# Performance work log

Measured on AMD Instinct MI355X. Metric: run time of the kernel, lower is better.

The kernel has to match this reference:

```python
import jax, jax.numpy as jnp
import numpy as np

B_SZ, SEQ, D_MODEL, N_STATE = 4, 2048, 768, 16


def setup_inputs() -> dict:
    key = jax.random.key(0)
    ks = jax.random.split(key, 8)
    s = 1.0 / np.sqrt(D_MODEL)
    x = jax.random.normal(ks[0], (B_SZ, SEQ, D_MODEL), dtype=jnp.float32)
    W1 = jax.random.uniform(ks[1], (D_MODEL, D_MODEL), jnp.float32, -s, s)
    b1 = jax.random.uniform(ks[2], (D_MODEL,), jnp.float32, -s, s)
    W2 = jax.random.uniform(ks[3], (D_MODEL, N_STATE), jnp.float32, -s, s)
    b2 = jax.random.uniform(ks[4], (N_STATE,), jnp.float32, -s, s)
    W3 = jax.random.uniform(ks[5], (D_MODEL, N_STATE), jnp.float32, -s, s)
    b3 = jax.random.uniform(ks[6], (N_STATE,), jnp.float32, -s, s)
    # A: xavier_uniform over (d_model, state_size)
    a_bound = np.sqrt(6.0 / (D_MODEL + N_STATE))
    A = jax.random.uniform(ks[7], (D_MODEL, N_STATE), jnp.float32, -a_bound, a_bound)
    return {"x": x, "W1": W1, "b1": b1, "W2": W2, "b2": b2, "W3": W3, "b3": b3, "A": A}


def reference(x, W1, b1, W2, b2, W3, b3, A):
    # Input-dependent projections
    Bm = x @ W2 + b2                     # [b, l, n]
    Cm = x @ W3 + b3                     # [b, l, n]
    delta = jax.nn.softplus(x @ W1 + b1)  # [b, l, d]
    # Discretization (S6)
    dB = delta[..., None] * Bm[:, :, None, :]                 # [b, l, d, n]
    dA = jnp.exp(jnp.einsum('bld,dn->bldn', delta, A))        # [b, l, d, n]
    # Source initializes h to zeros, so the dA*h term vanishes (no recurrence).
    h0 = jnp.zeros_like(dB)
    h = dA * h0 + x[..., None] * dB                            # [b, l, d, n]
    y = jnp.einsum('bln,bldn->bld', Cm, h)                     # [b, l, d]
    return y
```

## Files before the change

kernel.cpp:

```cpp
#include <hip/hip_runtime.h>
#include <hip/hip_bf16.h>
#include <math.h>


#define M_ROWS 8192
#define DM 768
#define NS 16

typedef short bf16x8 __attribute__((ext_vector_type(8)));
typedef float f32x4 __attribute__((ext_vector_type(4)));

__device__ __forceinline__ unsigned short f2bf(float f) {
    union { float f; unsigned u; } v; v.f = f;
    unsigned r = v.u + 0x7FFF + ((v.u >> 16) & 1);
    return (unsigned short)(r >> 16);
}
__device__ __forceinline__ float bf2f(unsigned short h) {
    union { unsigned u; float f; } v; v.u = ((unsigned)h) << 16; return v.f;
}
__device__ __forceinline__ void async16(const void* g, void* l) {
    __builtin_amdgcn_global_load_lds(
        (const __attribute__((address_space(1))) void*)g,
        (__attribute__((address_space(3))) void*)l,
        16, 0, 0);
}

__global__ __launch_bounds__(256) void prep_kernel(
    const float* __restrict__ x,
    const float* __restrict__ W1,
    const float* __restrict__ W2,
    const float* __restrict__ W3,
    unsigned short* __restrict__ xb,
    unsigned short* __restrict__ w1t,
    unsigned short* __restrict__ w23t)
{
    __shared__ float tile[32][33];
    const int bid = blockIdx.x;
    const int tid = threadIdx.x;
    if (bid < 32) {
        const int n = bid, i = n >> 1;
        const float* src = (n & 1) ? W3 : W2;
        #pragma unroll
        for (int e = 0; e < 3; ++e) {
            int k = e * 256 + tid;
            w23t[n * DM + k] = f2bf(src[k * NS + i]);
        }
    } else if (bid < 608) {
        const int b2i = bid - 32;
        const int n0 = (b2i % 24) * 32, k0 = (b2i / 24) * 32;
        const int tx = tid & 31, ty = tid >> 5;
        #pragma unroll
        for (int i = 0; i < 4; ++i) {
            int k = ty + i * 8;
            tile[k][tx] = W1[(k0 + k) * DM + n0 + tx];
        }
        __syncthreads();
        #pragma unroll
        for (int i = 0; i < 4; ++i) {
            int n = ty + i * 8;
            w1t[(n0 + n) * DM + k0 + tx] = f2bf(tile[tx][n]);
        }
    } else {
        int i = (bid - 608) * 256 + tid;
        float4 v = ((const float4*)x)[i];
        ushort4 o;
        o.x = f2bf(v.x); o.y = f2bf(v.y); o.z = f2bf(v.z); o.w = f2bf(v.w);
        ((ushort4*)xb)[i] = o;
    }
}

__global__ __launch_bounds__(256) void sgemm_kernel(
    const unsigned short* __restrict__ xb,
    const unsigned short* __restrict__ w23t,
    const float* __restrict__ b2, const float* __restrict__ b3,
    float* __restrict__ s_out)
{
    __shared__ unsigned short Al[64 * 64];
    __shared__ unsigned short Bl[32 * 64];
    const int m0 = blockIdx.x * 64;
    const int tid = threadIdx.x, lane = tid & 63, wave = tid >> 6;
    const int l15 = lane & 15, quad = lane >> 4;

    f32x4 acc[2];
    acc[0] = (f32x4){0.f,0.f,0.f,0.f};
    acc[1] = (f32x4){0.f,0.f,0.f,0.f};

    for (int k0 = 0; k0 < DM; k0 += 64) {
        #pragma unroll
        for (int i = 0; i < 2; ++i) {
            int ch = tid + i * 256;
            int r = ch >> 3, jg = (ch & 7) ^ (r & 7);
            async16(xb + (m0 + r) * DM + k0 + jg * 8, Al + ch * 8);
        }
        {
            int ch = tid;
            int r = ch >> 3, jg = (ch & 7) ^ (r & 7);
            async16(w23t + r * DM + k0 + jg * 8, Bl + ch * 8);
        }
        __syncthreads();
        #pragma unroll
        for (int kk = 0; kk < 2; ++kk) {
            int rr = wave * 16 + l15;
            int ja = (kk * 4 + quad) ^ (rr & 7);
            bf16x8 af = *(const bf16x8*)(Al + rr * 64 + ja * 8);
            #pragma unroll
            for (int t = 0; t < 2; ++t) {
                int rb = t * 16 + l15;
                int jb = (kk * 4 + quad) ^ (rb & 7);
                bf16x8 bfr = *(const bf16x8*)(Bl + rb * 64 + jb * 8);
                acc[t] = __builtin_amdgcn_mfma_f32_16x16x32_bf16(
                    af, bfr, acc[t], 0, 0, 0);
            }
        }
        __syncthreads();
    }

    float sacc[4] = {0.f, 0.f, 0.f, 0.f};
    #pragma unroll
    for (int t = 0; t < 2; ++t) {
        int p = t * 8 + (l15 >> 1);
        float bB = b2[p], bC = b3[p];
        #pragma unroll
        for (int r = 0; r < 4; ++r) {
            float v = acc[t][r];
            float pv = __shfl_xor(v, 1, 64);
            float term = (l15 & 1) ? (pv + bB) * (v + bC)
                                   : (v + bB) * (pv + bC);
            sacc[r] += term;
        }
    }
    #pragma unroll
    for (int r = 0; r < 4; ++r) {
        sacc[r] += __shfl_xor(sacc[r], 1, 64);
        sacc[r] += __shfl_xor(sacc[r], 2, 64);
        sacc[r] += __shfl_xor(sacc[r], 4, 64);
        sacc[r] += __shfl_xor(sacc[r], 8, 64);
    }
    if (l15 == 0) {
        #pragma unroll
        for (int r = 0; r < 4; ++r)
            s_out[m0 + wave * 16 + quad * 4 + r] = 0.5f * sacc[r];
    }
}

__global__ __launch_bounds__(256) void gemm_fused_kernel(
    const unsigned short* __restrict__ xb,
    const unsigned short* __restrict__ w1t,
    const float* __restrict__ b1,
    const float* __restrict__ s_arr,
    float* __restrict__ y)
{
    __shared__ unsigned short Al[128 * 64];
    __shared__ unsigned short Bl[64 * 64];
    const int b = blockIdx.x;
    const int c = b & 7, j = b >> 3;
    const int m0 = (c * 8 + j / 12) * 128;
    const int n0 = (j % 12) * 64;
    const int tid  = threadIdx.x;
    const int lane = tid & 63;
    const int wave = tid >> 6;
    const int wm = wave >> 1, wn = wave & 1;
    const int l15 = lane & 15, quad = lane >> 4;

    f32x4 acc[4][2];
    #pragma unroll
    for (int i = 0; i < 4; ++i)
        #pragma unroll
        for (int jj = 0; jj < 2; ++jj)
            acc[i][jj] = (f32x4){0.f, 0.f, 0.f, 0.f};

    for (int k0 = 0; k0 < DM; k0 += 64) {
        #pragma unroll
        for (int i = 0; i < 4; ++i) {
            int ch = tid + i * 256;
            int r = ch >> 3, jg = (ch & 7) ^ (r & 7);
            async16(xb + (m0 + r) * DM + k0 + jg * 8, Al + ch * 8);
        }
        #pragma unroll
        for (int i = 0; i < 2; ++i) {
            int ch = tid + i * 256;
            int r = ch >> 3, jg = (ch & 7) ^ (r & 7);
            async16(w1t + (n0 + r) * DM + k0 + jg * 8, Bl + ch * 8);
        }
        __syncthreads();

        #pragma unroll
        for (int kk = 0; kk < 2; ++kk) {
            bf16x8 bfr[2];
            #pragma unroll
            for (int jj = 0; jj < 2; ++jj) {
                int rb = wn * 32 + jj * 16 + l15;
                int jb = (kk * 4 + quad) ^ (rb & 7);
                bfr[jj] = *(const bf16x8*)(Bl + rb * 64 + jb * 8);
            }
            #pragma unroll
            for (int i = 0; i < 4; ++i) {
                int rr = wm * 64 + i * 16 + l15;
                int ja = (kk * 4 + quad) ^ (rr & 7);
                bf16x8 af = *(const bf16x8*)(Al + rr * 64 + ja * 8);
                #pragma unroll
                for (int jj = 0; jj < 2; ++jj)
                    acc[i][jj] = __builtin_amdgcn_mfma_f32_16x16x32_bf16(
                        af, bfr[jj], acc[i][jj], 0, 0, 0);
            }
        }
        __syncthreads();
    }

    #pragma unroll
    for (int i = 0; i < 4; ++i) {
        const int rowbase = m0 + wm * 64 + i * 16 + quad * 4;
        float4 s4 = *(const float4*)(s_arr + rowbase);
        #pragma unroll
        for (int jj = 0; jj < 2; ++jj) {
            int gcol = n0 + wn * 32 + jj * 16 + l15;
            float bias = b1[gcol];
            #pragma unroll
            for (int r = 0; r < 4; ++r) {
                int grow = rowbase + r;
                float v = acc[i][jj][r] + bias;
                float sp = (v > 20.f) ? v : log1pf(__expf(v));
                float xv = bf2f(xb[grow * DM + gcol]);
                float sv = (r == 0) ? s4.x : (r == 1) ? s4.y : (r == 2) ? s4.z : s4.w;
                y[grow * DM + gcol] = xv * sp * sv;
            }
        }
    }
}

extern "C" void kernel_launch(void* const* d_in, const int* in_sizes, int n_in,
                              void* d_out, int out_size, void* d_ws, size_t ws_size,
                              hipStream_t stream) {
    const float* x  = (const float*)d_in[0];
    const float* W1 = (const float*)d_in[1];
    const float* b1 = (const float*)d_in[2];
    const float* W2 = (const float*)d_in[3];
    const float* b2 = (const float*)d_in[4];
    const float* W3 = (const float*)d_in[5];
    const float* b3 = (const float*)d_in[6];
    float* y = (float*)d_out;

    unsigned short* xb   = (unsigned short*)d_ws;
    unsigned short* w1t  = (unsigned short*)((char*)d_ws + 12582912);
    unsigned short* w23t = (unsigned short*)((char*)d_ws + 13762560);
    float*          sarr = (float*)((char*)d_ws + 13811712);

    prep_kernel<<<6752, 256, 0, stream>>>(x, W1, W2, W3, xb, w1t, w23t);
    sgemm_kernel<<<128, 256, 0, stream>>>(xb, w23t, b2, b3, sarr);
    gemm_fused_kernel<<<768, 256, 0, stream>>>(xb, w1t, b1, sarr, y);
}
```

Measured before the change: 136.7 us.

## Double-buffer LDS tiles in main GEMM to overlap loads with MFMA

Splits the A and B shared-memory tiles of the fused W1 GEMM into two buffers. The first K-slice is loaded before the loop, and each iteration prefetches the next slice into the other buffer while MFMAs run on the current one. This leaves one barrier per iteration instead of two. The cost is doubled LDS use per block (48 KB), which may limit how many blocks fit on a CU. It also adds unused index variables.

```diff
diff --git a/kernel.cpp b/kernel.cpp
--- a/kernel.cpp
+++ b/kernel.cpp
@@ -150,8 +150,8 @@
     const float* __restrict__ s_arr,
     float* __restrict__ y)
 {
-    __shared__ unsigned short Al[128 * 64];
-    __shared__ unsigned short Bl[64 * 64];
+    __shared__ unsigned short Al[2][128 * 64];
+    __shared__ unsigned short Bl[2][64 * 64];
     const int b = blockIdx.x;
     const int c = b & 7, j = b >> 3;
     const int m0 = (c * 8 + j / 12) * 128;
@@ -162,6 +162,8 @@
     const int wm = wave >> 1, wn = wave & 1;
     const int l15 = lane & 15, quad = lane >> 4;
 
+    const int rA0 = tid >> 3, jA0 = (tid & 7) ^ (rA0 & 7);
+
     f32x4 acc[4][2];
     #pragma unroll
     for (int i = 0; i < 4; ++i)
@@ -169,20 +171,42 @@
         for (int jj = 0; jj < 2; ++jj)
             acc[i][jj] = (f32x4){0.f, 0.f, 0.f, 0.f};
 
-    for (int k0 = 0; k0 < DM; k0 += 64) {
+    {
+        const int k0 = 0;
         #pragma unroll
         for (int i = 0; i < 4; ++i) {
             int ch = tid + i * 256;
             int r = ch >> 3, jg = (ch & 7) ^ (r & 7);
-            async16(xb + (m0 + r) * DM + k0 + jg * 8, Al + ch * 8);
+            async16(xb + (m0 + r) * DM + k0 + jg * 8, &Al[0][ch * 8]);
         }
         #pragma unroll
         for (int i = 0; i < 2; ++i) {
             int ch = tid + i * 256;
             int r = ch >> 3, jg = (ch & 7) ^ (r & 7);
-            async16(w1t + (n0 + r) * DM + k0 + jg * 8, Bl + ch * 8);
-        }
-        __syncthreads();
+            async16(w1t + (n0 + r) * DM + k0 + jg * 8, &Bl[0][ch * 8]);
+        }
+    }
+
+    for (int step = 0; step < DM / 64; ++step) {
+        const int cur = step & 1;
+        __syncthreads();
+
+        if (step + 1 < DM / 64) {
+            const int k0 = (step + 1) * 64;
+            const int nxt = cur ^ 1;
+            #pragma unroll
+            for (int i = 0; i < 4; ++i) {
+                int ch = tid + i * 256;
+                int r = ch >> 3, jg = (ch & 7) ^ (r & 7);
+                async16(xb + (m0 + r) * DM + k0 + jg * 8, &Al[nxt][ch * 8]);
+            }
+            #pragma unroll
+            for (int i = 0; i < 2; ++i) {
+                int ch = tid + i * 256;
+                int r = ch >> 3, jg = (ch & 7) ^ (r & 7);
+                async16(w1t + (n0 + r) * DM + k0 + jg * 8, &Bl[nxt][ch * 8]);
+            }
+        }
 
         #pragma unroll
         for (int kk = 0; kk < 2; ++kk) {
@@ -191,20 +215,19 @@
             for (int jj = 0; jj < 2; ++jj) {
                 int rb = wn * 32 + jj * 16 + l15;
                 int jb = (kk * 4 + quad) ^ (rb & 7);
-                bfr[jj] = *(const bf16x8*)(Bl + rb * 64 + jb * 8);
+                bfr[jj] = *(const bf16x8*)(&Bl[cur][rb * 64 + jb * 8]);
             }
             #pragma unroll
             for (int i = 0; i < 4; ++i) {
                 int rr = wm * 64 + i * 16 + l15;
                 int ja = (kk * 4 + quad) ^ (rr & 7);
-                bf16x8 af = *(const bf16x8*)(Al + rr * 64 + ja * 8);
+                bf16x8 af = *(const bf16x8*)(&Al[cur][rr * 64 + ja * 8]);
                 #pragma unroll
                 for (int jj = 0; jj < 2; ++jj)
                     acc[i][jj] = __builtin_amdgcn_mfma_f32_16x16x32_bf16(
                         af, bfr[jj], acc[i][jj], 0, 0, 0);
             }
         }
-        __syncthreads();
     }
 
     #pragma unroll
@@ -226,6 +249,7 @@
             }
         }
     }
+    (void)rA0; (void)jA0;
 }
 
 extern "C" void kernel_launch(void* const* d_in, const int* in_sizes, int n_in,
```

Result: no change. 135.8 us (-0.7%).

## Fuse x conversion and state GEMM into prep; use two-wave 128x64 GEMM blocks

Applied to the files above, without the earlier changes.

The x-to-bf16 conversion and the small B/C projection GEMM now run in one kernel. Each block reads fp32 x directly, converts it in registers, writes xb and feeds it to MFMA while loading W2/W3 columns into LDS, which removes one launch and the extra xb read. The main GEMM now uses 128 threads (2 waves), each wave computing a 64x64 subtile with 16 accumulators and launch bounds of 3 blocks per SM, so each LDS B fragment is reused more. The risks are uncoalesced strided W2/W3 loads in every prep block, only 128 blocks doing the heavy x conversion, and fewer waves per block in the main GEMM to hide latency.

```diff
diff --git a/kernel.cpp b/kernel.cpp
--- a/kernel.cpp
+++ b/kernel.cpp
@@ -25,28 +25,99 @@
         16, 0, 0);
 }
 
-__global__ __launch_bounds__(256) void prep_kernel(
+__global__ __launch_bounds__(256) void prep_s_kernel(
     const float* __restrict__ x,
     const float* __restrict__ W1,
-    const float* __restrict__ W2,
-    const float* __restrict__ W3,
+    const float* __restrict__ W2, const float* __restrict__ b2,
+    const float* __restrict__ W3, const float* __restrict__ b3,
     unsigned short* __restrict__ xb,
     unsigned short* __restrict__ w1t,
-    unsigned short* __restrict__ w23t)
+    float* __restrict__ s_out)
 {
+    __shared__ unsigned short Bl[32 * 64];
     __shared__ float tile[32][33];
     const int bid = blockIdx.x;
     const int tid = threadIdx.x;
-    if (bid < 32) {
-        const int n = bid, i = n >> 1;
-        const float* src = (n & 1) ? W3 : W2;
-        #pragma unroll
-        for (int e = 0; e < 3; ++e) {
-            int k = e * 256 + tid;
-            w23t[n * DM + k] = f2bf(src[k * NS + i]);
-        }
-    } else if (bid < 608) {
-        const int b2i = bid - 32;
+
+    if (bid < 128) {
+        const int wave = tid >> 6, lane = tid & 63;
+        const int l15 = lane & 15, quad = lane >> 4;
+        const int rowbase = bid * 64 + wave * 16;
+        const int row = rowbase + l15;
+
+        const int sn = tid & 31;
+        const int skg = tid >> 5;
+        const float* wsrc = ((sn & 1) ? W3 : W2) + (sn >> 1);
+        const int sswz = skg ^ (sn & 7);
+
+        f32x4 acc[2];
+        acc[0] = (f32x4){0.f,0.f,0.f,0.f};
+        acc[1] = (f32x4){0.f,0.f,0.f,0.f};
+
+        for (int k0 = 0; k0 < DM; k0 += 64) {
+            {
+                float v[8];
+                #pragma unroll
+                for (int jj = 0; jj < 8; ++jj)
+                    v[jj] = wsrc[(k0 + skg * 8 + jj) * NS];
+                bf16x8 bv;
+                #pragma unroll
+                for (int jj = 0; jj < 8; ++jj)
+                    bv[jj] = (short)f2bf(v[jj]);
+                *(bf16x8*)(Bl + sn * 64 + sswz * 8) = bv;
+            }
+            __syncthreads();
+            #pragma unroll
+            for (int kk = 0; kk < 2; ++kk) {
+                const int kq = k0 + kk * 32 + quad * 8;
+                const float4* xp = (const float4*)(x + row * DM + kq);
+                float4 a0 = xp[0], a1 = xp[1];
+                bf16x8 af;
+                af[0] = (short)f2bf(a0.x); af[1] = (short)f2bf(a0.y);
+                af[2] = (short)f2bf(a0.z); af[3] = (short)f2bf(a0.w);
+                af[4] = (short)f2bf(a1.x); af[5] = (short)f2bf(a1.y);
+                af[6] = (short)f2bf(a1.z); af[7] = (short)f2bf(a1.w);
+                *(bf16x8*)(xb + row * DM + kq) = af;
+                #pragma unroll
+                for (int t = 0; t < 2; ++t) {
+                    int rb = t * 16 + l15;
+                    int jb = (kk * 4 + quad) ^ (rb & 7);
+                    bf16x8 bfr = *(const bf16x8*)(Bl + rb * 64 + jb * 8);
+                    acc[t] = __builtin_amdgcn_mfma_f32_16x16x32_bf16(
+                        af, bfr, acc[t], 0, 0, 0);
+                }
+            }
+            __syncthreads();
+        }
+
+        float sacc[4] = {0.f, 0.f, 0.f, 0.f};
+        #pragma unroll
+        for (int t = 0; t < 2; ++t) {
+            int p = t * 8 + (l15 >> 1);
+            float bB = b2[p], bC = b3[p];
+            #pragma unroll
+            for (int r = 0; r < 4; ++r) {
+                float v = acc[t][r];
+                float pv = __shfl_xor(v, 1, 64);
+                float term = (l15 & 1) ? (pv + bB) * (v + bC)
+                                       : (v + bB) * (pv + bC);
+                sacc[r] += term;
+            }
+        }
+        #pragma unroll
+        for (int r = 0; r < 4; ++r) {
+            sacc[r] += __shfl_xor(sacc[r], 1, 64);
+            sacc[r] += __shfl_xor(sacc[r], 2, 64);
+            sacc[r] += __shfl_xor(sacc[r], 4, 64);
+            sacc[r] += __shfl_xor(sacc[r], 8, 64);
+        }
+        if (l15 == 0) {
+            #pragma unroll
+            for (int r = 0; r < 4; ++r)
+                s_out[rowbase + quad * 4 + r] = 0.5f * sacc[r];
+        }
+    } else {
+        const int b2i = bid - 128;
         const int n0 = (b2i % 24) * 32, k0 = (b2i / 24) * 32;
         const int tx = tid & 31, ty = tid >> 5;
         #pragma unroll
@@ -60,90 +131,10 @@
             int n = ty + i * 8;
             w1t[(n0 + n) * DM + k0 + tx] = f2bf(tile[tx][n]);
         }
-    } else {
-        int i = (bid - 608) * 256 + tid;
-        float4 v = ((const float4*)x)[i];
-        ushort4 o;
-        o.x = f2bf(v.x); o.y = f2bf(v.y); o.z = f2bf(v.z); o.w = f2bf(v.w);
-        ((ushort4*)xb)[i] = o;
     }
 }
 
-__global__ __launch_bounds__(256) void sgemm_kernel(
-    const unsigned short* __restrict__ xb,
-    const unsigned short* __restrict__ w23t,
-    const float* __restrict__ b2, const float* __restrict__ b3,
-    float* __restrict__ s_out)
-{
-    __shared__ unsigned short Al[64 * 64];
-    __shared__ unsigned short Bl[32 * 64];
-    const int m0 = blockIdx.x * 64;
-    const int tid = threadIdx.x, lane = tid & 63, wave = tid >> 6;
-    const int l15 = lane & 15, quad = lane >> 4;
-
-    f32x4 acc[2];
-    acc[0] = (f32x4){0.f,0.f,0.f,0.f};
-    acc[1] = (f32x4){0.f,0.f,0.f,0.f};
-
-    for (int k0 = 0; k0 < DM; k0 += 64) {
-        #pragma unroll
-        for (int i = 0; i < 2; ++i) {
-            int ch = tid + i * 256;
-            int r = ch >> 3, jg = (ch & 7) ^ (r & 7);
-            async16(xb + (m0 + r) * DM + k0 + jg * 8, Al + ch * 8);
-        }
-        {
-            int ch = tid;
-            int r = ch >> 3, jg = (ch & 7) ^ (r & 7);
-            async16(w23t + r * DM + k0 + jg * 8, Bl + ch * 8);
-        }
-        __syncthreads();
-        #pragma unroll
-        for (int kk = 0; kk < 2; ++kk) {
-            int rr = wave * 16 + l15;
-            int ja = (kk * 4 + quad) ^ (rr & 7);
-            bf16x8 af = *(const bf16x8*)(Al + rr * 64 + ja * 8);
-            #pragma unroll
-            for (int t = 0; t < 2; ++t) {
-                int rb = t * 16 + l15;
-                int jb = (kk * 4 + quad) ^ (rb & 7);
-                bf16x8 bfr = *(const bf16x8*)(Bl + rb * 64 + jb * 8);
-                acc[t] = __builtin_amdgcn_mfma_f32_16x16x32_bf16(
-                    af, bfr, acc[t], 0, 0, 0);
-            }
-        }
-        __syncthreads();
-    }
-
-    float sacc[4] = {0.f, 0.f, 0.f, 0.f};
-    #pragma unroll
-    for (int t = 0; t < 2; ++t) {
-        int p = t * 8 + (l15 >> 1);
-        float bB = b2[p], bC = b3[p];
-        #pragma unroll
-        for (int r = 0; r < 4; ++r) {
-            float v = acc[t][r];
-            float pv = __shfl_xor(v, 1, 64);
-            float term = (l15 & 1) ? (pv + bB) * (v + bC)
-                                   : (v + bB) * (pv + bC);
-            sacc[r] += term;
-        }
-    }
-    #pragma unroll
-    for (int r = 0; r < 4; ++r) {
-        sacc[r] += __shfl_xor(sacc[r], 1, 64);
-        sacc[r] += __shfl_xor(sacc[r], 2, 64);
-        sacc[r] += __shfl_xor(sacc[r], 4, 64);
-        sacc[r] += __shfl_xor(sacc[r], 8, 64);
-    }
-    if (l15 == 0) {
-        #pragma unroll
-        for (int r = 0; r < 4; ++r)
-            s_out[m0 + wave * 16 + quad * 4 + r] = 0.5f * sacc[r];
-    }
-}
-
-__global__ __launch_bounds__(256) void gemm_fused_kernel(
+__global__ __launch_bounds__(128, 3) void gemm_fused_kernel(
     const unsigned short* __restrict__ xb,
     const unsigned short* __restrict__ w1t,
     const float* __restrict__ b1,
@@ -158,27 +149,26 @@
     const int n0 = (j % 12) * 64;
     const int tid  = threadIdx.x;
     const int lane = tid & 63;
-    const int wave = tid >> 6;
-    const int wm = wave >> 1, wn = wave & 1;
+    const int w    = tid >> 6;
     const int l15 = lane & 15, quad = lane >> 4;
 
-    f32x4 acc[4][2];
+    f32x4 acc[4][4];
     #pragma unroll
     for (int i = 0; i < 4; ++i)
         #pragma unroll
-        for (int jj = 0; jj < 2; ++jj)
+        for (int jj = 0; jj < 4; ++jj)
             acc[i][jj] = (f32x4){0.f, 0.f, 0.f, 0.f};
 
     for (int k0 = 0; k0 < DM; k0 += 64) {
         #pragma unroll
-        for (int i = 0; i < 4; ++i) {
-            int ch = tid + i * 256;
+        for (int i = 0; i < 8; ++i) {
+            int ch = tid + i * 128;
             int r = ch >> 3, jg = (ch & 7) ^ (r & 7);
             async16(xb + (m0 + r) * DM + k0 + jg * 8, Al + ch * 8);
         }
         #pragma unroll
-        for (int i = 0; i < 2; ++i) {
-            int ch = tid + i * 256;
+        for (int i = 0; i < 4; ++i) {
+            int ch = tid + i * 128;
             int r = ch >> 3, jg = (ch & 7) ^ (r & 7);
             async16(w1t + (n0 + r) * DM + k0 + jg * 8, Bl + ch * 8);
         }
@@ -186,20 +176,20 @@
 
         #pragma unroll
         for (int kk = 0; kk < 2; ++kk) {
-            bf16x8 bfr[2];
-            #pragma unroll
-            for (int jj = 0; jj < 2; ++jj) {
-                int rb = wn * 32 + jj * 16 + l15;
+            bf16x8 bfr[4];
+            #pragma unroll
+            for (int jj = 0; jj < 4; ++jj) {
+                int rb = jj * 16 + l15;
                 int jb = (kk * 4 + quad) ^ (rb & 7);
                 bfr[jj] = *(const bf16x8*)(Bl + rb * 64 + jb * 8);
             }
             #pragma unroll
             for (int i = 0; i < 4; ++i) {
-                int rr = wm * 64 + i * 16 + l15;
+                int rr = w * 64 + i * 16 + l15;
                 int ja = (kk * 4 + quad) ^ (rr & 7);
                 bf16x8 af = *(const bf16x8*)(Al + rr * 64 + ja * 8);
                 #pragma unroll
-                for (int jj = 0; jj < 2; ++jj)
+                for (int jj = 0; jj < 4; ++jj)
                     acc[i][jj] = __builtin_amdgcn_mfma_f32_16x16x32_bf16(
                         af, bfr[jj], acc[i][jj], 0, 0, 0);
             }
@@ -209,11 +199,11 @@
 
     #pragma unroll
     for (int i = 0; i < 4; ++i) {
-        const int rowbase = m0 + wm * 64 + i * 16 + quad * 4;
+        const int rowbase = m0 + w * 64 + i * 16 + quad * 4;
         float4 s4 = *(const float4*)(s_arr + rowbase);
         #pragma unroll
-        for (int jj = 0; jj < 2; ++jj) {
-            int gcol = n0 + wn * 32 + jj * 16 + l15;
+        for (int jj = 0; jj < 4; ++jj) {
+            int gcol = n0 + jj * 16 + l15;
             float bias = b1[gcol];
             #pragma unroll
             for (int r = 0; r < 4; ++r) {
@@ -242,10 +232,9 @@
 
     unsigned short* xb   = (unsigned short*)d_ws;
     unsigned short* w1t  = (unsigned short*)((char*)d_ws + 12582912);
-    unsigned short* w23t = (unsigned short*)((char*)d_ws + 13762560);
-    float*          sarr = (float*)((char*)d_ws + 13811712);
-
-    prep_kernel<<<6752, 256, 0, stream>>>(x, W1, W2, W3, xb, w1t, w23t);
-    sgemm_kernel<<<128, 256, 0, stream>>>(xb, w23t, b2, b3, sarr);
-    gemm_fused_kernel<<<768, 256, 0, stream>>>(xb, w1t, b1, sarr, y);
-}
+    float*          sarr = (float*)((char*)d_ws + 13762560);
+
+    prep_s_kernel<<<704, 256, 0, stream>>>(x, W1, W2, b2, W3, b3,
+                                           xb, w1t, sarr);
+    gemm_fused_kernel<<<768, 128, 0, stream>>>(xb, w1t, b1, sarr, y);
+}
```

Result: slower. 152.4 us (+11.4%).
